# Performance work log

Hardware: AMD Instinct MI355X
Metric: run time of the kernel (lower is better)

Reference implementation:

```python
import jax, jax.numpy as jnp
import numpy as np

EMBED_DIM = 768
NUM_HEADS = 12
HEAD_DIM = EMBED_DIM // NUM_HEADS
IMG_LEN = 196
TXT_LEN = 1852
SEQ_LEN = IMG_LEN + TXT_LEN
BATCH = 4
NEG = -1e9


def setup_inputs() -> dict:
    key = jax.random.key(0)
    ks = jax.random.split(key, 10)
    s = 1.0 / np.sqrt(EMBED_DIM)
    return {
        "x": jax.random.normal(ks[0], (BATCH, SEQ_LEN, EMBED_DIM), jnp.float32),
        "input_padding_mask": jax.random.randint(ks[1], (BATCH, TXT_LEN), 0, 2, jnp.int32),
        "Wq": jax.random.normal(ks[2], (EMBED_DIM, EMBED_DIM), jnp.float32) * s,
        "bq": jax.random.normal(ks[3], (EMBED_DIM,), jnp.float32) * 0.01,
        "Wk": jax.random.normal(ks[4], (EMBED_DIM, EMBED_DIM), jnp.float32) * s,
        "bk": jax.random.normal(ks[5], (EMBED_DIM,), jnp.float32) * 0.01,
        "Wv": jax.random.normal(ks[6], (EMBED_DIM, EMBED_DIM), jnp.float32) * s,
        "bv": jax.random.normal(ks[7], (EMBED_DIM,), jnp.float32) * 0.01,
        "Wo": jax.random.normal(ks[8], (EMBED_DIM, EMBED_DIM), jnp.float32) * s,
        "bo": jax.random.normal(ks[9], (EMBED_DIM,), jnp.float32) * 0.01,
    }


def _prefix_causal_mask():
    # tril ones, but all rows fully attend to the image prefix columns
    m = jnp.tril(jnp.ones((SEQ_LEN, SEQ_LEN), jnp.float32))
    m = m.at[:, :IMG_LEN].set(1.0)
    return m


def reference(x, input_padding_mask, Wq, bq, Wk, bk, Wv, bv, Wo, bo):
    B, S, E = x.shape
    H, D = NUM_HEADS, HEAD_DIM
    # torch nn.Linear: y = x @ W.T + b, weight shape [out, in]
    q = (x @ Wq.T + bq).reshape(B, S, H, D).transpose(0, 2, 1, 3)  # [B,H,S,D]
    k = (x @ Wk.T + bk).reshape(B, S, H, D).transpose(0, 2, 1, 3)
    v = (x @ Wv.T + bv).reshape(B, S, H, D).transpose(0, 2, 1, 3)

    sims = jnp.einsum("bhqd,bhkd->bhqk", q, k) / jnp.sqrt(jnp.float32(D))
    mask = _prefix_causal_mask()[None, None]  # [1,1,S,S]
    sims = jnp.where(mask == 0, NEG, sims)

    # padding mask over key positions (image prefix always valid)
    full_pad = jnp.concatenate(
        [jnp.ones((B, IMG_LEN), input_padding_mask.dtype), input_padding_mask], axis=1
    )  # [B,S]
    sims = jnp.where(full_pad[:, None, None, :] == 0, NEG, sims)

    attn = jax.nn.softmax(sims, axis=-1)
    out = jnp.einsum("bhqk,bhkd->bhqd", attn, v)
    out = out.transpose(0, 2, 1, 3).reshape(B, S, E)
    return out @ Wo.T + bo
```

## Files before the change

kernel.cpp:

```cpp
#include <hip/hip_runtime.h>

#define B_ 4
#define S_ 2048
#define E_ 768
#define H_ 12
#define D_ 64
#define IMG_ 196
#define TXT_ 1852
#define NEG_ (-1e9f)

typedef __bf16 bf16x8 __attribute__((ext_vector_type(8)));
typedef float f32x4 __attribute__((ext_vector_type(4)));
typedef float f32x16 __attribute__((ext_vector_type(16)));

__device__ __forceinline__ unsigned short f2b(float f) {
    __bf16 h = (__bf16)f;
    return __builtin_bit_cast(unsigned short, h);
}
__device__ __forceinline__ unsigned int pack2(float lo, float hi) {
    return (unsigned int)f2b(lo) | ((unsigned int)f2b(hi) << 16);
}
__device__ __forceinline__ void gload16(const unsigned short* g, unsigned short* l) {
    __builtin_amdgcn_global_load_lds(
        (const __attribute__((address_space(1))) unsigned int*)g,
        (__attribute__((address_space(3))) unsigned int*)l, 16, 0, 0);
}


__global__ __launch_bounds__(256) void cvt_kernel(const float* __restrict__ src,
                                                  unsigned short* __restrict__ dst,
                                                  int n4) {
    int i = blockIdx.x * 256 + threadIdx.x;
    if (i < n4) {
        float4 f = reinterpret_cast<const float4*>(src)[i];
        ushort4 u;
        u.x = f2b(f.x); u.y = f2b(f.y); u.z = f2b(f.z); u.w = f2b(f.w);
        reinterpret_cast<ushort4*>(dst)[i] = u;
    }
}

__global__ __launch_bounds__(256) void padneg_kernel(const int* __restrict__ pad,
                                                     float* __restrict__ padneg) {
    int i = blockIdx.x * 256 + threadIdx.x;
    if (i < B_ * S_) {
        int b = i >> 11, s = i & 2047;
        float v = 0.f;
        if (s >= IMG_) v = pad[b * TXT_ + (s - IMG_)] ? 0.f : NEG_;
        padneg[i] = v;
    }
}

__global__ __launch_bounds__(256) void qkv_gemm(
    const unsigned short* __restrict__ xb,
    const unsigned short* __restrict__ wqb,
    const unsigned short* __restrict__ wkb,
    const unsigned short* __restrict__ wvb,
    const float* __restrict__ bq, const float* __restrict__ bk,
    const float* __restrict__ bv,
    unsigned short* __restrict__ qfb, unsigned short* __restrict__ kfb,
    unsigned short* __restrict__ vfb)
{
    __shared__ __align__(16) unsigned short As[128 * 64];
    __shared__ __align__(16) unsigned short Bs[128 * 64];
    const int m0 = blockIdx.x * 128;
    const int n0 = blockIdx.y * 128;
    const int which = n0 / E_;
    const int ncol0 = n0 % E_;
    const unsigned short* W = (which == 0) ? wqb : ((which == 1) ? wkb : wvb);
    const int t = threadIdx.x;
    const int lane = t & 63, wid = t >> 6;
    const int wr = wid >> 1, wc = wid & 1;
    const int c = lane & 15, g = lane >> 4;
    const int srow = lane >> 3;
    const int sslot = (lane & 7) ^ srow;

    f32x4 acc[4][4];
#pragma unroll
    for (int i = 0; i < 4; ++i)
#pragma unroll
        for (int j = 0; j < 4; ++j) acc[i][j] = (f32x4){0.f, 0.f, 0.f, 0.f};

    for (int k0 = 0; k0 < E_; k0 += 64) {
        __syncthreads();
#pragma unroll
        for (int j = 0; j < 8; ++j) {
            int chunk = wid * 8 + j;
            int isB = chunk >> 4;
            int ch = chunk & 15;
            int row = ch * 8 + srow;
            const unsigned short* src =
                (isB ? W + (size_t)(ncol0 + row) * E_
                     : xb + (size_t)(m0 + row) * E_) + k0 + sslot * 8;
            unsigned short* dst = (isB ? Bs : As) + ch * 512;
            gload16(src, dst);
        }
        __syncthreads();

        bf16x8 af[2][4], bfv[2][4];
#pragma unroll
        for (int kk = 0; kk < 2; ++kk) {
#pragma unroll
            for (int fr = 0; fr < 4; ++fr) {
                int row = wr * 64 + fr * 16 + c;
                af[kk][fr] = *reinterpret_cast<const bf16x8*>(
                    &As[row * 64 + (((kk * 4 + g) ^ (row & 7)) * 8)]);
            }
#pragma unroll
            for (int fc = 0; fc < 4; ++fc) {
                int row = wc * 64 + fc * 16 + c;
                bfv[kk][fc] = *reinterpret_cast<const bf16x8*>(
                    &Bs[row * 64 + (((kk * 4 + g) ^ (row & 7)) * 8)]);
            }
        }
#pragma unroll
        for (int kk = 0; kk < 2; ++kk)
#pragma unroll
            for (int fr = 0; fr < 4; ++fr)
#pragma unroll
                for (int fc = 0; fc < 4; ++fc)
                    acc[fr][fc] = __builtin_amdgcn_mfma_f32_16x16x32_bf16(
                        af[kk][fr], bfv[kk][fc], acc[fr][fc], 0, 0, 0);
    }

    const float* bias_ptr = (which == 0) ? bq : ((which == 1) ? bk : bv);
    if (which != 2) {
        unsigned short* dstbuf = (which == 0) ? qfb : kfb;
#pragma unroll
        for (int fc = 0; fc < 4; ++fc) {
            int e = ncol0 + wc * 64 + fc * 16 + c;
            float bias = bias_ptr[e];
            int hd = e >> 6, d = e & 63;
            int dc = d >> 4, hf = (d >> 3) & 1, e8 = d & 7;
#pragma unroll
            for (int fr = 0; fr < 4; ++fr) {
#pragma unroll
                for (int r = 0; r < 4; ++r) {
                    int m = m0 + wr * 64 + fr * 16 + g * 4 + r;
                    int b = m >> 11, s = m & 2047;
                    int bh = b * H_ + hd, t32 = s >> 5, sl = s & 31;
                    size_t off = ((((size_t)bh * 64 + t32) * 4 + dc) * 64
                                  + hf * 32 + sl) * 8 + e8;
                    dstbuf[off] = f2b(acc[fr][fc][r] + bias);
                }
            }
        }
    } else {
#pragma unroll
        for (int fc = 0; fc < 4; ++fc) {
            int e = ncol0 + wc * 64 + fc * 16 + c;
            float bias = bias_ptr[e];
            int hd = e >> 6, d = e & 63;
            int vh = d >> 5, dl = d & 31;
#pragma unroll
            for (int fr = 0; fr < 4; ++fr) {
                int m = m0 + wr * 64 + fr * 16 + g * 4;
                int b = m >> 11, s = m & 2047;
                int bh = b * H_ + hd, t32 = s >> 5, ks = s & 31;
                int mm = ks >> 4, hb = (ks >> 3) & 1, e8 = ks & 7;
                size_t off = (((((size_t)bh * 64 + t32) * 2 + mm) * 2 + vh) * 64
                              + hb * 32 + dl) * 8 + e8;
                uint2 pk;
                pk.x = pack2(acc[fr][fc][0] + bias, acc[fr][fc][1] + bias);
                pk.y = pack2(acc[fr][fc][2] + bias, acc[fr][fc][3] + bias);
                *reinterpret_cast<uint2*>(&vfb[off]) = pk;
            }
        }
    }
}

__global__ __launch_bounds__(256) void attn_kernel(
    const unsigned short* __restrict__ qfb,
    const unsigned short* __restrict__ kfb,
    const unsigned short* __restrict__ vfb,
    const float* __restrict__ padneg,
    unsigned short* __restrict__ ob)
{
    __shared__ float pneg[S_];
    __shared__ float exch[2][34][64];
    const int flat = blockIdx.x;
    const int xcd = flat & 7, idx = flat >> 3;
    const int bh = xcd * 6 + (idx >> 5);
    const int qg = idx & 31;
    const int b = bh / H_, hh = bh % H_;
    const int t = threadIdx.x;

    {
        const float4* src = reinterpret_cast<const float4*>(padneg + b * S_);
        float4* dst = reinterpret_cast<float4*>(pneg);
        dst[t] = src[t];
        dst[t + 256] = src[t + 256];
    }
    __syncthreads();

    const int lane = t & 63, w = t >> 6;
    const int h = lane >> 5, ql = lane & 31;
    const int taskid = w >> 1, half = w & 1;
    const int qt = taskid ? (63 - qg) : qg;
    const int qbase = qt * 32;
    const int q = qbase + ql;

    bf16x8 qf[4];
    {
        const unsigned short* qp = qfb + ((size_t)(bh * 64 + qt) * 4) * 512 + lane * 8;
#pragma unroll
        for (int dc = 0; dc < 4; ++dc)
            qf[dc] = *reinterpret_cast<const bf16x8*>(qp + dc * 512);
    }

    f32x16 oa0, oa1;
#pragma unroll
    for (int r = 0; r < 16; ++r) { oa0[r] = 0.f; oa1[r] = 0.f; }
    float mr = -3.0e38f, lr = 0.f;

    int kmax = qbase + 32; if (kmax < IMG_) kmax = IMG_;
    const int nt = (kmax + 31) >> 5;

    for (int kt = half; kt < nt; kt += 2) {
        const int k0 = kt * 32;
        bf16x8 kf[4];
        {
            const unsigned short* kp = kfb + ((size_t)(bh * 64 + kt) * 4) * 512 + lane * 8;
#pragma unroll
            for (int dc = 0; dc < 4; ++dc)
                kf[dc] = *reinterpret_cast<const bf16x8*>(kp + dc * 512);
        }

        f32x16 s;
#pragma unroll
        for (int r = 0; r < 16; ++r) s[r] = 0.f;
#pragma unroll
        for (int dc = 0; dc < 4; ++dc)
            s = __builtin_amdgcn_mfma_f32_32x32x16_bf16(kf[dc], qf[dc], s, 0, 0, 0);

        float pna[16];
        *reinterpret_cast<float4*>(&pna[0])  = *reinterpret_cast<const float4*>(&pneg[k0 + 0  + 4 * h]);
        *reinterpret_cast<float4*>(&pna[4])  = *reinterpret_cast<const float4*>(&pneg[k0 + 8  + 4 * h]);
        *reinterpret_cast<float4*>(&pna[8])  = *reinterpret_cast<const float4*>(&pneg[k0 + 16 + 4 * h]);
        *reinterpret_cast<float4*>(&pna[12]) = *reinterpret_cast<const float4*>(&pneg[k0 + 24 + 4 * h]);
#pragma unroll
        for (int r = 0; r < 16; ++r) s[r] = fmaf(s[r], 0.125f, pna[r]);

        if (kt == nt - 1) {
#pragma unroll
            for (int r = 0; r < 16; ++r) {
                int key = k0 + (r & 3) + 8 * (r >> 2) + 4 * h;
                if (!((key <= q) || (key < IMG_))) s[r] = NEG_;
            }
        }

        float t0 = fmaxf(fmaxf(s[0], s[1]), fmaxf(s[2], s[3]));
        float t1 = fmaxf(fmaxf(s[4], s[5]), fmaxf(s[6], s[7]));
        float t2 = fmaxf(fmaxf(s[8], s[9]), fmaxf(s[10], s[11]));
        float t3 = fmaxf(fmaxf(s[12], s[13]), fmaxf(s[14], s[15]));
        float tm = fmaxf(fmaxf(t0, t1), fmaxf(t2, t3));
        tm = fmaxf(tm, __shfl_xor(tm, 32, 64));

        if (!__all(tm - mr <= 8.f)) {
            float mnew = fmaxf(mr, tm);
            float alpha = __expf(mr - mnew);
            mr = mnew; lr *= alpha;
#pragma unroll
            for (int r = 0; r < 16; ++r) { oa0[r] *= alpha; oa1[r] *= alpha; }
        }

        float p[16];
#pragma unroll
        for (int r = 0; r < 16; ++r) p[r] = __expf(s[r] - mr);
        float a0 = (p[0] + p[1]) + (p[2] + p[3]);
        float a1 = (p[4] + p[5]) + (p[6] + p[7]);
        float a2 = (p[8] + p[9]) + (p[10] + p[11]);
        float a3 = (p[12] + p[13]) + (p[14] + p[15]);
        float ss = (a0 + a1) + (a2 + a3);
        ss += __shfl_xor(ss, 32, 64);
        lr += ss;

        unsigned int pka0 = pack2(p[0], p[1]),   pkb0 = pack2(p[2], p[3]);
        unsigned int pka1 = pack2(p[4], p[5]),   pkb1 = pack2(p[6], p[7]);
        unsigned int pka2 = pack2(p[8], p[9]),   pkb2 = pack2(p[10], p[11]);
        unsigned int pka3 = pack2(p[12], p[13]), pkb3 = pack2(p[14], p[15]);

        const unsigned short* vp = vfb + ((size_t)(bh * 64 + kt) * 4) * 512 + lane * 8;
#pragma unroll
        for (int m = 0; m < 2; ++m) {
            unsigned int keep0 = h ? (m ? pka3 : pka1) : (m ? pka2 : pka0);
            unsigned int keep1 = h ? (m ? pkb3 : pkb1) : (m ? pkb2 : pkb0);
            unsigned int send0 = h ? (m ? pka2 : pka0) : (m ? pka3 : pka1);
            unsigned int send1 = h ? (m ? pkb2 : pkb0) : (m ? pkb3 : pkb1);
            unsigned int x0 = (unsigned int)__shfl_xor((int)send0, 32, 64);
            unsigned int x1 = (unsigned int)__shfl_xor((int)send1, 32, 64);
            uint4 fr;
            fr.x = h ? x0 : keep0;
            fr.y = h ? x1 : keep1;
            fr.z = h ? keep0 : x0;
            fr.w = h ? keep1 : x1;
            bf16x8 pb = __builtin_bit_cast(bf16x8, fr);
            bf16x8 vf0 = *reinterpret_cast<const bf16x8*>(vp + (m * 2 + 0) * 512);
            bf16x8 vf1 = *reinterpret_cast<const bf16x8*>(vp + (m * 2 + 1) * 512);
            oa0 = __builtin_amdgcn_mfma_f32_32x32x16_bf16(vf0, pb, oa0, 0, 0, 0);
            oa1 = __builtin_amdgcn_mfma_f32_32x32x16_bf16(vf1, pb, oa1, 0, 0, 0);
        }
    }

    float* X = &exch[taskid][0][0];
    if (half) {
#pragma unroll
        for (int r = 0; r < 16; ++r) {
            X[r * 64 + lane] = oa0[r];
            X[(16 + r) * 64 + lane] = oa1[r];
        }
        X[32 * 64 + lane] = mr;
        X[33 * 64 + lane] = lr;
    }
    __syncthreads();
    if (half) return;

    float m1 = X[32 * 64 + lane], l1 = X[33 * 64 + lane];
    float mnew = fmaxf(mr, m1);
    float w0 = __expf(mr - mnew), w1 = __expf(m1 - mnew);
    float inv = 1.f / (lr * w0 + l1 * w1);

    unsigned short* orow = ob + ((size_t)(b * S_ + q)) * E_ + hh * D_;
#pragma unroll
    for (int gg = 0; gg < 4; ++gg) {
        int d0 = gg * 8 + 4 * h;
        float v0[4], v1[4];
#pragma unroll
        for (int j = 0; j < 4; ++j) {
            int r = 4 * gg + j;
            v0[j] = (oa0[r] * w0 + X[r * 64 + lane] * w1) * inv;
            v1[j] = (oa1[r] * w0 + X[(16 + r) * 64 + lane] * w1) * inv;
        }
        uint2 s0, s1;
        s0.x = pack2(v0[0], v0[1]); s0.y = pack2(v0[2], v0[3]);
        s1.x = pack2(v1[0], v1[1]); s1.y = pack2(v1[2], v1[3]);
        *reinterpret_cast<uint2*>(orow + d0) = s0;
        *reinterpret_cast<uint2*>(orow + 32 + d0) = s1;
    }
}

__global__ __launch_bounds__(256) void oproj_gemm(
    const unsigned short* __restrict__ ab,
    const unsigned short* __restrict__ wob,
    const float* __restrict__ bo,
    float* __restrict__ out)
{
    __shared__ __align__(16) unsigned short As[128 * 64];
    __shared__ __align__(16) unsigned short Bs[128 * 64];
    const int m0 = blockIdx.x * 128;
    const int n0 = blockIdx.y * 128;
    const int t = threadIdx.x;
    const int lane = t & 63, wid = t >> 6;
    const int wr = wid >> 1, wc = wid & 1;
    const int c = lane & 15, g = lane >> 4;
    const int srow = lane >> 3;
    const int sslot = (lane & 7) ^ srow;

    f32x4 acc[4][4];
#pragma unroll
    for (int i = 0; i < 4; ++i)
#pragma unroll
        for (int j = 0; j < 4; ++j) acc[i][j] = (f32x4){0.f, 0.f, 0.f, 0.f};

    for (int k0 = 0; k0 < E_; k0 += 64) {
        __syncthreads();
#pragma unroll
        for (int j = 0; j < 8; ++j) {
            int chunk = wid * 8 + j;
            int isB = chunk >> 4;
            int ch = chunk & 15;
            int row = ch * 8 + srow;
            const unsigned short* src =
                (isB ? wob + (size_t)(n0 + row) * E_
                     : ab + (size_t)(m0 + row) * E_) + k0 + sslot * 8;
            unsigned short* dst = (isB ? Bs : As) + ch * 512;
            gload16(src, dst);
        }
        __syncthreads();

        bf16x8 af[2][4], bfv[2][4];
#pragma unroll
        for (int kk = 0; kk < 2; ++kk) {
#pragma unroll
            for (int fr = 0; fr < 4; ++fr) {
                int row = wr * 64 + fr * 16 + c;
                af[kk][fr] = *reinterpret_cast<const bf16x8*>(
                    &As[row * 64 + (((kk * 4 + g) ^ (row & 7)) * 8)]);
            }
#pragma unroll
            for (int fc = 0; fc < 4; ++fc) {
                int row = wc * 64 + fc * 16 + c;
                bfv[kk][fc] = *reinterpret_cast<const bf16x8*>(
                    &Bs[row * 64 + (((kk * 4 + g) ^ (row & 7)) * 8)]);
            }
        }
#pragma unroll
        for (int kk = 0; kk < 2; ++kk)
#pragma unroll
            for (int fr = 0; fr < 4; ++fr)
#pragma unroll
                for (int fc = 0; fc < 4; ++fc)
                    acc[fr][fc] = __builtin_amdgcn_mfma_f32_16x16x32_bf16(
                        af[kk][fr], bfv[kk][fc], acc[fr][fc], 0, 0, 0);
    }

#pragma unroll
    for (int fc = 0; fc < 4; ++fc) {
        int n = n0 + wc * 64 + fc * 16 + c;
        float bias = bo[n];
#pragma unroll
        for (int fr = 0; fr < 4; ++fr)
#pragma unroll
            for (int r = 0; r < 4; ++r) {
                int m = m0 + wr * 64 + fr * 16 + g * 4 + r;
                out[(size_t)m * E_ + n] = acc[fr][fc][r] + bias;
            }
    }
}

extern "C" void kernel_launch(void* const* d_in, const int* in_sizes, int n_in,
                              void* d_out, int out_size, void* d_ws, size_t ws_size,
                              hipStream_t stream) {
    const float* x  = (const float*)d_in[0];
    const int* pad  = (const int*)d_in[1];
    const float* Wq = (const float*)d_in[2];
    const float* bq = (const float*)d_in[3];
    const float* Wk = (const float*)d_in[4];
    const float* bk = (const float*)d_in[5];
    const float* Wv = (const float*)d_in[6];
    const float* bv = (const float*)d_in[7];
    const float* Wo = (const float*)d_in[8];
    const float* bo = (const float*)d_in[9];
    float* out = (float*)d_out;

    const size_t NX = (size_t)B_ * S_ * E_;
    const size_t NW = (size_t)E_ * E_;
    unsigned short* ws = (unsigned short*)d_ws;
    unsigned short* xb  = ws;
    unsigned short* wqb = xb + NX;
    unsigned short* wkb = wqb + NW;
    unsigned short* wvb = wkb + NW;
    unsigned short* wob = wvb + NW;
    unsigned short* qfb = wob + NW;
    unsigned short* kfb = qfb + NX;
    unsigned short* vfb = kfb + NX;
    unsigned short* obuf = vfb + NX;
    float* padneg = (float*)(obuf + NX);

    cvt_kernel<<<(int)(NX / 4 / 256), 256, 0, stream>>>(x, xb, (int)(NX / 4));
    cvt_kernel<<<(int)(NW / 4 / 256), 256, 0, stream>>>(Wq, wqb, (int)(NW / 4));
    cvt_kernel<<<(int)(NW / 4 / 256), 256, 0, stream>>>(Wk, wkb, (int)(NW / 4));
    cvt_kernel<<<(int)(NW / 4 / 256), 256, 0, stream>>>(Wv, wvb, (int)(NW / 4));
    cvt_kernel<<<(int)(NW / 4 / 256), 256, 0, stream>>>(Wo, wob, (int)(NW / 4));
    padneg_kernel<<<(B_ * S_) / 256, 256, 0, stream>>>(pad, padneg);

    qkv_gemm<<<dim3(64, 18), 256, 0, stream>>>(xb, wqb, wkb, wvb, bq, bk, bv,
                                               qfb, kfb, vfb);
    attn_kernel<<<dim3(1536), 256, 0, stream>>>(qfb, kfb, vfb, padneg, obuf);
    oproj_gemm<<<dim3(64, 6), 256, 0, stream>>>(obuf, wob, bo, out);
}
```

Measured before the change: 169.1 us.

## Give each attention wave its own query tile and drop split-KV merging

Attention blocks now handle four consecutive query tiles, one per wave, instead of two paired (light/heavy) tiles each split across two waves by alternating key tiles. This removes the LDS exchange, the extra barrier and the merge of partial softmax states. The key loop processes two key tiles per iteration for more MFMA independence, and only the last tile applies the causal mask. The four weight conversions are also fused into one launch. The risk is load imbalance: waves within a block get different causal lengths, blocks differ in total work, and the grid shrinks to 768 blocks.

```diff
diff --git a/kernel.cpp b/kernel.cpp
--- a/kernel.cpp
+++ b/kernel.cpp
@@ -37,6 +37,23 @@
         u.x = f2b(f.x); u.y = f2b(f.y); u.z = f2b(f.z); u.w = f2b(f.w);
         reinterpret_cast<ushort4*>(dst)[i] = u;
     }
+}
+
+__global__ __launch_bounds__(256) void cvtw_kernel(
+    const float* __restrict__ w0, const float* __restrict__ w1,
+    const float* __restrict__ w2, const float* __restrict__ w3,
+    unsigned short* __restrict__ d0, unsigned short* __restrict__ d1,
+    unsigned short* __restrict__ d2, unsigned short* __restrict__ d3,
+    int n4) {
+    int i = blockIdx.x * 256 + threadIdx.x;
+    if (i >= n4) return;
+    int which = blockIdx.y;
+    const float* src = (which == 0) ? w0 : (which == 1) ? w1 : (which == 2) ? w2 : w3;
+    unsigned short* dst = (which == 0) ? d0 : (which == 1) ? d1 : (which == 2) ? d2 : d3;
+    float4 f = reinterpret_cast<const float4*>(src)[i];
+    ushort4 u;
+    u.x = f2b(f.x); u.y = f2b(f.y); u.z = f2b(f.z); u.w = f2b(f.w);
+    reinterpret_cast<ushort4*>(dst)[i] = u;
 }
 
 __global__ __launch_bounds__(256) void padneg_kernel(const int* __restrict__ pad,
@@ -169,18 +186,17 @@
 }
 
 __global__ __launch_bounds__(256) void attn_kernel(
-    const unsigned short* __restrict__ qfb,
-    const unsigned short* __restrict__ kfb,
-    const unsigned short* __restrict__ vfb,
+    const unsigned short* __restrict__ qF,
+    const unsigned short* __restrict__ kF,
+    const unsigned short* __restrict__ vF,
     const float* __restrict__ padneg,
     unsigned short* __restrict__ ob)
 {
     __shared__ float pneg[S_];
-    __shared__ float exch[2][34][64];
     const int flat = blockIdx.x;
     const int xcd = flat & 7, idx = flat >> 3;
-    const int bh = xcd * 6 + (idx >> 5);
-    const int qg = idx & 31;
+    const int bh = xcd * 6 + (idx >> 4);
+    const int qgroup = idx & 15;
     const int b = bh / H_, hh = bh % H_;
     const int t = threadIdx.x;
 
@@ -194,14 +210,13 @@
 
     const int lane = t & 63, w = t >> 6;
     const int h = lane >> 5, ql = lane & 31;
-    const int taskid = w >> 1, half = w & 1;
-    const int qt = taskid ? (63 - qg) : qg;
+    const int qt = qgroup * 4 + w;
     const int qbase = qt * 32;
     const int q = qbase + ql;
 
     bf16x8 qf[4];
     {
-        const unsigned short* qp = qfb + ((size_t)(bh * 64 + qt) * 4) * 512 + lane * 8;
+        const unsigned short* qp = qF + ((size_t)(bh * 64 + qt) * 4) * 512 + lane * 8;
 #pragma unroll
         for (int dc = 0; dc < 4; ++dc)
             qf[dc] = *reinterpret_cast<const bf16x8*>(qp + dc * 512);
@@ -214,72 +229,17 @@
 
     int kmax = qbase + 32; if (kmax < IMG_) kmax = IMG_;
     const int nt = (kmax + 31) >> 5;
-
-    for (int kt = half; kt < nt; kt += 2) {
-        const int k0 = kt * 32;
-        bf16x8 kf[4];
-        {
-            const unsigned short* kp = kfb + ((size_t)(bh * 64 + kt) * 4) * 512 + lane * 8;
-#pragma unroll
-            for (int dc = 0; dc < 4; ++dc)
-                kf[dc] = *reinterpret_cast<const bf16x8*>(kp + dc * 512);
-        }
-
-        f32x16 s;
-#pragma unroll
-        for (int r = 0; r < 16; ++r) s[r] = 0.f;
-#pragma unroll
-        for (int dc = 0; dc < 4; ++dc)
-            s = __builtin_amdgcn_mfma_f32_32x32x16_bf16(kf[dc], qf[dc], s, 0, 0, 0);
-
-        float pna[16];
-        *reinterpret_cast<float4*>(&pna[0])  = *reinterpret_cast<const float4*>(&pneg[k0 + 0  + 4 * h]);
-        *reinterpret_cast<float4*>(&pna[4])  = *reinterpret_cast<const float4*>(&pneg[k0 + 8  + 4 * h]);
-        *reinterpret_cast<float4*>(&pna[8])  = *reinterpret_cast<const float4*>(&pneg[k0 + 16 + 4 * h]);
-        *reinterpret_cast<float4*>(&pna[12]) = *reinterpret_cast<const float4*>(&pneg[k0 + 24 + 4 * h]);
-#pragma unroll
-        for (int r = 0; r < 16; ++r) s[r] = fmaf(s[r], 0.125f, pna[r]);
-
-        if (kt == nt - 1) {
-#pragma unroll
-            for (int r = 0; r < 16; ++r) {
-                int key = k0 + (r & 3) + 8 * (r >> 2) + 4 * h;
-                if (!((key <= q) || (key < IMG_))) s[r] = NEG_;
-            }
-        }
-
-        float t0 = fmaxf(fmaxf(s[0], s[1]), fmaxf(s[2], s[3]));
-        float t1 = fmaxf(fmaxf(s[4], s[5]), fmaxf(s[6], s[7]));
-        float t2 = fmaxf(fmaxf(s[8], s[9]), fmaxf(s[10], s[11]));
-        float t3 = fmaxf(fmaxf(s[12], s[13]), fmaxf(s[14], s[15]));
-        float tm = fmaxf(fmaxf(t0, t1), fmaxf(t2, t3));
-        tm = fmaxf(tm, __shfl_xor(tm, 32, 64));
-
-        if (!__all(tm - mr <= 8.f)) {
-            float mnew = fmaxf(mr, tm);
-            float alpha = __expf(mr - mnew);
-            mr = mnew; lr *= alpha;
-#pragma unroll
-            for (int r = 0; r < 16; ++r) { oa0[r] *= alpha; oa1[r] *= alpha; }
-        }
-
-        float p[16];
-#pragma unroll
-        for (int r = 0; r < 16; ++r) p[r] = __expf(s[r] - mr);
-        float a0 = (p[0] + p[1]) + (p[2] + p[3]);
-        float a1 = (p[4] + p[5]) + (p[6] + p[7]);
-        float a2 = (p[8] + p[9]) + (p[10] + p[11]);
-        float a3 = (p[12] + p[13]) + (p[14] + p[15]);
-        float ss = (a0 + a1) + (a2 + a3);
-        ss += __shfl_xor(ss, 32, 64);
-        lr += ss;
-
+    const int npre = nt - 1;
+
+    const unsigned short* kbase = kF + ((size_t)bh * 64 * 4) * 512 + lane * 8;
+    const unsigned short* vbase = vF + ((size_t)bh * 64 * 4) * 512 + lane * 8;
+
+    auto pvstep = [&](const f32x16& p, int tile) {
         unsigned int pka0 = pack2(p[0], p[1]),   pkb0 = pack2(p[2], p[3]);
         unsigned int pka1 = pack2(p[4], p[5]),   pkb1 = pack2(p[6], p[7]);
         unsigned int pka2 = pack2(p[8], p[9]),   pkb2 = pack2(p[10], p[11]);
         unsigned int pka3 = pack2(p[12], p[13]), pkb3 = pack2(p[14], p[15]);
-
-        const unsigned short* vp = vfb + ((size_t)(bh * 64 + kt) * 4) * 512 + lane * 8;
+        const unsigned short* vp = vbase + (size_t)tile * 2048;
 #pragma unroll
         for (int m = 0; m < 2; ++m) {
             unsigned int keep0 = h ? (m ? pka3 : pka1) : (m ? pka2 : pka0);
@@ -299,40 +259,123 @@
             oa0 = __builtin_amdgcn_mfma_f32_32x32x16_bf16(vf0, pb, oa0, 0, 0, 0);
             oa1 = __builtin_amdgcn_mfma_f32_32x32x16_bf16(vf1, pb, oa1, 0, 0, 0);
         }
-    }
-
-    float* X = &exch[taskid][0][0];
-    if (half) {
+    };
+
+    auto loadpna = [&](float* pna, int k0) {
+        *reinterpret_cast<float4*>(&pna[0])  = *reinterpret_cast<const float4*>(&pneg[k0 + 0  + 4 * h]);
+        *reinterpret_cast<float4*>(&pna[4])  = *reinterpret_cast<const float4*>(&pneg[k0 + 8  + 4 * h]);
+        *reinterpret_cast<float4*>(&pna[8])  = *reinterpret_cast<const float4*>(&pneg[k0 + 16 + 4 * h]);
+        *reinterpret_cast<float4*>(&pna[12]) = *reinterpret_cast<const float4*>(&pneg[k0 + 24 + 4 * h]);
+    };
+
+    int kt = 0;
+    for (; kt + 2 <= npre; kt += 2) {
+        const unsigned short* kpa = kbase + (size_t)kt * 2048;
+        bf16x8 ka[4], kb4[4];
+#pragma unroll
+        for (int dc = 0; dc < 4; ++dc) {
+            ka[dc]  = *reinterpret_cast<const bf16x8*>(kpa + dc * 512);
+            kb4[dc] = *reinterpret_cast<const bf16x8*>(kpa + 2048 + dc * 512);
+        }
+        f32x16 sa, sb;
+#pragma unroll
+        for (int r = 0; r < 16; ++r) { sa[r] = 0.f; sb[r] = 0.f; }
+#pragma unroll
+        for (int dc = 0; dc < 4; ++dc) {
+            sa = __builtin_amdgcn_mfma_f32_32x32x16_bf16(ka[dc],  qf[dc], sa, 0, 0, 0);
+            sb = __builtin_amdgcn_mfma_f32_32x32x16_bf16(kb4[dc], qf[dc], sb, 0, 0, 0);
+        }
+        float pna[16], pnb[16];
+        loadpna(pna, kt * 32);
+        loadpna(pnb, kt * 32 + 32);
 #pragma unroll
         for (int r = 0; r < 16; ++r) {
-            X[r * 64 + lane] = oa0[r];
-            X[(16 + r) * 64 + lane] = oa1[r];
-        }
-        X[32 * 64 + lane] = mr;
-        X[33 * 64 + lane] = lr;
-    }
-    __syncthreads();
-    if (half) return;
-
-    float m1 = X[32 * 64 + lane], l1 = X[33 * 64 + lane];
-    float mnew = fmaxf(mr, m1);
-    float w0 = __expf(mr - mnew), w1 = __expf(m1 - mnew);
-    float inv = 1.f / (lr * w0 + l1 * w1);
-
+            sa[r] = fmaf(sa[r], 0.125f, pna[r]);
+            sb[r] = fmaf(sb[r], 0.125f, pnb[r]);
+        }
+        float tm = fmaxf(sa[0], sb[0]);
+#pragma unroll
+        for (int r = 1; r < 16; ++r) tm = fmaxf(tm, fmaxf(sa[r], sb[r]));
+        tm = fmaxf(tm, __shfl_xor(tm, 32, 64));
+        if (!__all(tm - mr <= 8.f)) {
+            float mnew = fmaxf(mr, tm);
+            float alpha = __expf(mr - mnew);
+            mr = mnew; lr *= alpha;
+#pragma unroll
+            for (int r = 0; r < 16; ++r) { oa0[r] *= alpha; oa1[r] *= alpha; }
+        }
+#pragma unroll
+        for (int r = 0; r < 16; ++r) {
+            sa[r] = __expf(sa[r] - mr);
+            sb[r] = __expf(sb[r] - mr);
+        }
+        float ss = 0.f;
+#pragma unroll
+        for (int r = 0; r < 16; ++r) ss += sa[r] + sb[r];
+        ss += __shfl_xor(ss, 32, 64);
+        lr += ss;
+        pvstep(sa, kt);
+        pvstep(sb, kt + 1);
+    }
+
+#pragma unroll 1
+    for (int pass = (npre & 1) ? 0 : 1; pass < 2; ++pass) {
+        const int tile = pass ? (nt - 1) : (npre - 1);
+        const bool causal = (pass == 1);
+        const unsigned short* kp = kbase + (size_t)tile * 2048;
+        bf16x8 kf4[4];
+#pragma unroll
+        for (int dc = 0; dc < 4; ++dc)
+            kf4[dc] = *reinterpret_cast<const bf16x8*>(kp + dc * 512);
+        f32x16 s;
+#pragma unroll
+        for (int r = 0; r < 16; ++r) s[r] = 0.f;
+#pragma unroll
+        for (int dc = 0; dc < 4; ++dc)
+            s = __builtin_amdgcn_mfma_f32_32x32x16_bf16(kf4[dc], qf[dc], s, 0, 0, 0);
+        const int k0 = tile * 32;
+        float pna[16];
+        loadpna(pna, k0);
+#pragma unroll
+        for (int r = 0; r < 16; ++r) s[r] = fmaf(s[r], 0.125f, pna[r]);
+        if (causal) {
+#pragma unroll
+            for (int r = 0; r < 16; ++r) {
+                int key = k0 + (r & 3) + 8 * (r >> 2) + 4 * h;
+                if (!((key <= q) || (key < IMG_))) s[r] = NEG_;
+            }
+        }
+        float tm = s[0];
+#pragma unroll
+        for (int r = 1; r < 16; ++r) tm = fmaxf(tm, s[r]);
+        tm = fmaxf(tm, __shfl_xor(tm, 32, 64));
+        if (!__all(tm - mr <= 8.f)) {
+            float mnew = fmaxf(mr, tm);
+            float alpha = __expf(mr - mnew);
+            mr = mnew; lr *= alpha;
+#pragma unroll
+            for (int r = 0; r < 16; ++r) { oa0[r] *= alpha; oa1[r] *= alpha; }
+        }
+#pragma unroll
+        for (int r = 0; r < 16; ++r) s[r] = __expf(s[r] - mr);
+        float ss = 0.f;
+#pragma unroll
+        for (int r = 0; r < 16; ++r) ss += s[r];
+        ss += __shfl_xor(ss, 32, 64);
+        lr += ss;
+        pvstep(s, tile);
+    }
+
+    float inv = 1.f / lr;
     unsigned short* orow = ob + ((size_t)(b * S_ + q)) * E_ + hh * D_;
 #pragma unroll
     for (int gg = 0; gg < 4; ++gg) {
         int d0 = gg * 8 + 4 * h;
-        float v0[4], v1[4];
-#pragma unroll
-        for (int j = 0; j < 4; ++j) {
-            int r = 4 * gg + j;
-            v0[j] = (oa0[r] * w0 + X[r * 64 + lane] * w1) * inv;
-            v1[j] = (oa1[r] * w0 + X[(16 + r) * 64 + lane] * w1) * inv;
-        }
         uint2 s0, s1;
-        s0.x = pack2(v0[0], v0[1]); s0.y = pack2(v0[2], v0[3]);
-        s1.x = pack2(v1[0], v1[1]); s1.y = pack2(v1[2], v1[3]);
+        s0.x = pack2(oa0[4 * gg] * inv, oa0[4 * gg + 1] * inv);
+        s0.y = pack2(oa0[4 * gg + 2] * inv, oa0[4 * gg + 3] * inv);
+        s1.x = pack2(oa1[4 * gg] * inv, oa1[4 * gg + 1] * inv);
+        s1.y = pack2(oa1[4 * gg + 2] * inv, oa1[4 * gg + 3] * inv);
         *reinterpret_cast<uint2*>(orow + d0) = s0;
         *reinterpret_cast<uint2*>(orow + 32 + d0) = s1;
     }
@@ -447,14 +490,12 @@
     float* padneg = (float*)(obuf + NX);
 
     cvt_kernel<<<(int)(NX / 4 / 256), 256, 0, stream>>>(x, xb, (int)(NX / 4));
-    cvt_kernel<<<(int)(NW / 4 / 256), 256, 0, stream>>>(Wq, wqb, (int)(NW / 4));
-    cvt_kernel<<<(int)(NW / 4 / 256), 256, 0, stream>>>(Wk, wkb, (int)(NW / 4));
-    cvt_kernel<<<(int)(NW / 4 / 256), 256, 0, stream>>>(Wv, wvb, (int)(NW / 4));
-    cvt_kernel<<<(int)(NW / 4 / 256), 256, 0, stream>>>(Wo, wob, (int)(NW / 4));
+    cvtw_kernel<<<dim3((int)(NW / 4 / 256), 4), 256, 0, stream>>>(
+        Wq, Wk, Wv, Wo, wqb, wkb, wvb, wob, (int)(NW / 4));
     padneg_kernel<<<(B_ * S_) / 256, 256, 0, stream>>>(pad, padneg);
 
     qkv_gemm<<<dim3(64, 18), 256, 0, stream>>>(xb, wqb, wkb, wvb, bq, bk, bv,
                                                qfb, kfb, vfb);
-    attn_kernel<<<dim3(1536), 256, 0, stream>>>(qfb, kfb, vfb, padneg, obuf);
+    attn_kernel<<<dim3(768), 256, 0, stream>>>(qfb, kfb, vfb, padneg, obuf);
     oproj_gemm<<<dim3(64, 6), 256, 0, stream>>>(obuf, wob, bo, out);
 }
```

After: 173.7 us. +2.7%, slower.
